# Performance work log

Measured on AMD Instinct MI355X. Metric: run time of the kernel, lower is better.

Reference implementation:

```python
import jax, jax.numpy as jnp
import numpy as np
from jax import lax

PATCH = 3
RBF_SIGMA = 0.06 * PATCH ** 2      # module scales sigma by patch_size**2
SIG2 = RBF_SIGMA ** 2


def _unfold(img):
    # torch.nn.Unfold(kernel_size=3, stride=1): (b, c*9, N) with N=(H-2)*(W-2).
    # Channel ordering inside d differs from torch but distances sum over d,
    # so any consistent patch flattening yields identical math.
    p = lax.conv_general_dilated_patches(img, (PATCH, PATCH), (1, 1), 'VALID')
    b, d = p.shape[0], p.shape[1]
    return p.reshape(b, d, -1)  # (b, d, N)


def _kernel_mean(xu, yu):
    # mean over (N, M) of exp(-||x_i - y_j||^2 / sigma^2), via the
    # ||x||^2 + ||y||^2 - 2<x,y> expansion (avoids the (b,d,N,M) diff tensor).
    sqx = jnp.sum(xu * xu, axis=1)                   # (b, N)
    sqy = jnp.sum(yu * yu, axis=1)                   # (b, M)
    gram = jnp.einsum('bdn,bdm->bnm', xu, yu)        # (b, N, M)
    d2 = sqx[:, :, None] + sqy[:, None, :] - 2.0 * gram
    return jnp.mean(jnp.exp(-d2 / SIG2), axis=(1, 2))  # (b,)


def setup_inputs() -> dict:
    key = jax.random.key(0)
    kx, ky = jax.random.split(key)
    x = jax.random.normal(kx, (8, 3, 64, 64), dtype=jnp.float32)
    y = jax.random.normal(ky, (8, 3, 64, 64), dtype=jnp.float32)
    return {"x": x, "y": y}


def reference(x, y):
    xu = _unfold(x)
    yu = _unfold(y)
    batch_loss = (-2.0 * _kernel_mean(xu, yu)
                  + _kernel_mean(xu, xu)
                  + _kernel_mean(yu, yu))       # (b,)
    return jnp.mean(batch_loss)                 # batch_reduction='mean'
```

## Files before the change

kernel.cpp:

```cpp
#include <hip/hip_runtime.h>
#include <hip/hip_bf16.h>


#define NP    3844
#define NPAD  3968
#define KP    32

#define W_XY  7688
#define W_ALL 15624
#define NBLK  15624

static constexpr float L_F   = 4.9475824173972215f;
static constexpr float C2L_F = 9.895164834794443f;

using bf16x8 = __attribute__((ext_vector_type(8))) short;
using f32x4  = __attribute__((ext_vector_type(4))) float;

#define MFMA16(a, b, c) __builtin_amdgcn_mfma_f32_16x16x32_bf16((a), (b), (c), 0, 0, 0)

__device__ inline unsigned short f2bf(float f) {
    union { float f; unsigned u; } v; v.f = f;
    unsigned r = v.u + 0x7FFFu + ((v.u >> 16) & 1u);
    return (unsigned short)(r >> 16);
}
__device__ inline float bf2f(unsigned short h) {
    union { unsigned u; float f; } v; v.u = ((unsigned)h) << 16;
    return v.f;
}
__device__ inline void pack_store(unsigned short* dst, const unsigned short* v) {
    uint4* d = (uint4*)dst;
#pragma unroll
    for (int q = 0; q < 4; ++q) {
        unsigned w0 = (unsigned)v[8 * q + 0] | ((unsigned)v[8 * q + 1] << 16);
        unsigned w1 = (unsigned)v[8 * q + 2] | ((unsigned)v[8 * q + 3] << 16);
        unsigned w2 = (unsigned)v[8 * q + 4] | ((unsigned)v[8 * q + 5] << 16);
        unsigned w3 = (unsigned)v[8 * q + 6] | ((unsigned)v[8 * q + 7] << 16);
        d[q] = make_uint4(w0, w1, w2, w3);
    }
}

__global__ __launch_bounds__(256) void gp_prep(const float* __restrict__ x,
                                               const float* __restrict__ y,
                                               unsigned short* __restrict__ Am,
                                               unsigned short* __restrict__ Bm) {
    int i = blockIdx.x * 256 + threadIdx.x;
    if (i >= 16 * NPAD) return;
    int n = i % NPAD, im = i / NPAD;
    int b = im & 7;
    const float* src = (im >> 3) ? y : x;

    const unsigned short ONE = f2bf(1.0f);
    unsigned short hA[32], hB[32];
#pragma unroll
    for (int k = 0; k < 32; ++k) { hA[k] = 0; hB[k] = 0; }

    if (n < NP) {
        int r = n / 62, c = n % 62;
        float s = 0.0f;
#pragma unroll
        for (int ch = 0; ch < 3; ++ch)
#pragma unroll
            for (int pr = 0; pr < 3; ++pr)
#pragma unroll
                for (int pc = 0; pc < 3; ++pc) {
                    int k = ch * 9 + pr * 3 + pc;
                    float v = src[(((b * 3 + ch) * 64) + r + pr) * 64 + (c + pc)];
                    unsigned short ah = f2bf(C2L_F * v);
                    unsigned short bh = f2bf(v);
                    hA[k] = ah; hB[k] = bh;
                    s = fmaf(bf2f(ah), bf2f(bh), s);
                }
        float p = -0.5f * s;
        hA[27] = f2bf(p); hA[28] = f2bf(p - bf2f(hA[27]));
        hA[29] = ONE; hA[30] = ONE;
        hB[27] = ONE; hB[28] = ONE;
        hB[29] = f2bf(p); hB[30] = f2bf(p - bf2f(hB[29]));
    } else {
        hA[27] = f2bf(-1e30f); hA[29] = ONE; hA[30] = ONE;
        hB[27] = ONE; hB[28] = ONE; hB[29] = f2bf(-1e30f);
    }

    pack_store(Am + (size_t)i * KP, hA);
    pack_store(Bm + (size_t)i * KP, hB);
}

template<int OFF>
__device__ inline bf16x8 gload(const unsigned short* p) {
    bf16x8 r;
    asm volatile("global_load_dwordx4 %0, %1, off offset:%2"
                 : "=v"(r) : "v"(p), "i"(OFF));
    return r;
}

#define BODY(BHC)                                                            \
    do {                                                                     \
        const f32x4 Z = {0.f, 0.f, 0.f, 0.f};                                \
        f32x4 g0 = MFMA16(ah0, BHC, Z); f32x4 g1 = MFMA16(ah1, BHC, Z);      \
        f32x4 g2 = MFMA16(ah2, BHC, Z); f32x4 g3 = MFMA16(ah3, BHC, Z);      \
        f32x4 g4 = MFMA16(ah4, BHC, Z); f32x4 g5 = MFMA16(ah5, BHC, Z);      \
        f32x4 g6 = MFMA16(ah6, BHC, Z); f32x4 g7 = MFMA16(ah7, BHC, Z);      \
        float m0 = fmaxf(fmaxf(fmaxf(g0[0], g0[1]), g0[2]), g0[3]);          \
        float m1 = fmaxf(fmaxf(fmaxf(g1[0], g1[1]), g1[2]), g1[3]);          \
        float m2 = fmaxf(fmaxf(fmaxf(g2[0], g2[1]), g2[2]), g2[3]);          \
        float m3 = fmaxf(fmaxf(fmaxf(g3[0], g3[1]), g3[2]), g3[3]);          \
        float m4 = fmaxf(fmaxf(fmaxf(g4[0], g4[1]), g4[2]), g4[3]);          \
        float m5 = fmaxf(fmaxf(fmaxf(g5[0], g5[1]), g5[2]), g5[3]);          \
        float m6 = fmaxf(fmaxf(fmaxf(g6[0], g6[1]), g6[2]), g6[3]);          \
        float m7 = fmaxf(fmaxf(fmaxf(g7[0], g7[1]), g7[2]), g7[3]);          \
        float mm = fmaxf(fmaxf(fmaxf(fmaxf(fmaxf(fmaxf(fmaxf(m0, m1), m2),   \
                         m3), m4), m5), m6), m7);                            \
        if (__any(mm > -40.0f)) {                                            \
            s0 += __builtin_amdgcn_exp2f(g0[0]); s1 += __builtin_amdgcn_exp2f(g0[1]); \
            s2 += __builtin_amdgcn_exp2f(g0[2]); s3 += __builtin_amdgcn_exp2f(g0[3]); \
            s0 += __builtin_amdgcn_exp2f(g1[0]); s1 += __builtin_amdgcn_exp2f(g1[1]); \
            s2 += __builtin_amdgcn_exp2f(g1[2]); s3 += __builtin_amdgcn_exp2f(g1[3]); \
            s0 += __builtin_amdgcn_exp2f(g2[0]); s1 += __builtin_amdgcn_exp2f(g2[1]); \
            s2 += __builtin_amdgcn_exp2f(g2[2]); s3 += __builtin_amdgcn_exp2f(g2[3]); \
            s0 += __builtin_amdgcn_exp2f(g3[0]); s1 += __builtin_amdgcn_exp2f(g3[1]); \
            s2 += __builtin_amdgcn_exp2f(g3[2]); s3 += __builtin_amdgcn_exp2f(g3[3]); \
            s0 += __builtin_amdgcn_exp2f(g4[0]); s1 += __builtin_amdgcn_exp2f(g4[1]); \
            s2 += __builtin_amdgcn_exp2f(g4[2]); s3 += __builtin_amdgcn_exp2f(g4[3]); \
            s0 += __builtin_amdgcn_exp2f(g5[0]); s1 += __builtin_amdgcn_exp2f(g5[1]); \
            s2 += __builtin_amdgcn_exp2f(g5[2]); s3 += __builtin_amdgcn_exp2f(g5[3]); \
            s0 += __builtin_amdgcn_exp2f(g6[0]); s1 += __builtin_amdgcn_exp2f(g6[1]); \
            s2 += __builtin_amdgcn_exp2f(g6[2]); s3 += __builtin_amdgcn_exp2f(g6[3]); \
            s0 += __builtin_amdgcn_exp2f(g7[0]); s1 += __builtin_amdgcn_exp2f(g7[1]); \
            s2 += __builtin_amdgcn_exp2f(g7[2]); s3 += __builtin_amdgcn_exp2f(g7[3]); \
        }                                                                    \
    } while (0)

#define STEPN(N, CURREG)                                                     \
    do {                                                                     \
        asm volatile("s_waitcnt vmcnt(" #N ")" : "+v"(CURREG));              \
        __builtin_amdgcn_sched_barrier(0);                                   \
        BODY(CURREG);                                                        \
    } while (0)

__global__ __launch_bounds__(64, 4) void gp_pairs21(const unsigned short* __restrict__ Am,
                                                    const unsigned short* __restrict__ Bm,
                                                    float* __restrict__ part) {
    const int phys = blockIdx.x;
    const int w = (phys & 7) * 1953 + (phys >> 3);

    const int l = threadIdx.x & 63;
    const int l15 = l & 15, lhi = l >> 4;

    int type, b, bx, by;
    float wt;
    if (w < W_XY) {
        type = 0; b = w / 961;
        int rr = w % 961; by = rr / 31; bx = rr % 31;
        wt = -2.0f;
    } else {
        int v = w - W_XY;
        type = 1 + v / 3968;
        int r = v % 3968; b = r / 496; int t2 = r % 496;
        by = (int)((sqrtf(8.0f * (float)t2 + 1.0f) - 1.0f) * 0.5f);
        while ((by + 1) * (by + 2) / 2 <= t2) ++by;
        while (by * (by + 1) / 2 > t2) --by;
        bx = t2 - by * (by + 1) / 2;
        wt = (bx == by) ? 1.0f : 2.0f;
    }
    int imA, imB;
    if (type == 0)      { imA = b;     imB = 8 + b; }
    else if (type == 1) { imA = b;     imB = b;     }
    else                { imA = 8 + b; imB = 8 + b; }

    const size_t eA = ((size_t)(imA * NPAD + bx * 128 + l15)) * KP + lhi * 8;
    const size_t eB = ((size_t)(imB * NPAD + by * 128 + l15)) * KP + lhi * 8;
    const unsigned short* pA0 = Am + eA;
    const unsigned short* pA4 = pA0 + 2048;
    const unsigned short* pB0 = Bm + eB;
    const unsigned short* pB4 = pB0 + 2048;

    bf16x8 ah0 = gload<0>(pA0),    ah1 = gload<1024>(pA0);
    bf16x8 ah2 = gload<2048>(pA0), ah3 = gload<3072>(pA0);
    bf16x8 ah4 = gload<0>(pA4),    ah5 = gload<1024>(pA4);
    bf16x8 ah6 = gload<2048>(pA4), ah7 = gload<3072>(pA4);

    bf16x8 b0 = gload<0>(pB0),    b1 = gload<1024>(pB0);
    bf16x8 b2 = gload<2048>(pB0), b3 = gload<3072>(pB0);
    bf16x8 b4 = gload<0>(pB4),    b5 = gload<1024>(pB4);
    bf16x8 b6 = gload<2048>(pB4), b7 = gload<3072>(pB4);

    asm volatile("s_waitcnt vmcnt(8)"
                 : "+v"(ah0), "+v"(ah1), "+v"(ah2), "+v"(ah3),
                   "+v"(ah4), "+v"(ah5), "+v"(ah6), "+v"(ah7));
    __builtin_amdgcn_sched_barrier(0);

    float s0 = 0.f, s1 = 0.f, s2 = 0.f, s3 = 0.f;

    STEPN(7, b0);
    STEPN(6, b1);
    STEPN(5, b2);
    STEPN(4, b3);
    STEPN(3, b4);
    STEPN(2, b5);
    STEPN(1, b6);
    STEPN(0, b7);

    float sacc = wt * ((s0 + s1) + (s2 + s3));

#pragma unroll
    for (int o = 32; o > 0; o >>= 1) sacc += __shfl_down(sacc, o, 64);
    if (l == 0) part[w] = sacc;
}

__global__ __launch_bounds__(1024) void gp_finish(const float* __restrict__ part,
                                                  float* __restrict__ out) {
    __shared__ float red[16];
    const int t = threadIdx.x;
    const int wv = t >> 6, l = t & 63;

    float s = 0.0f;
    for (int i = t; i < W_ALL; i += 1024) s += part[i];
#pragma unroll
    for (int o = 32; o > 0; o >>= 1) s += __shfl_down(s, o, 64);
    if (l == 0) red[wv] = s;
    __syncthreads();
    if (t == 0) {
        double d = 0.0;
#pragma unroll
        for (int i = 0; i < 16; ++i) d += (double)red[i];
        out[0] = (float)(d / (8.0 * (double)NP * (double)NP));
    }
}

extern "C" void kernel_launch(void* const* d_in, const int* in_sizes, int n_in,
                              void* d_out, int out_size, void* d_ws, size_t ws_size,
                              hipStream_t stream) {
    const float* x = (const float*)d_in[0];
    const float* y = (const float*)d_in[1];
    const size_t MSZ = (size_t)16 * NPAD * KP;
    unsigned short* Am = (unsigned short*)d_ws;
    unsigned short* Bm = Am + MSZ;
    float* part = (float*)(Bm + MSZ);

    gp_prep<<<(16 * NPAD) / 256, 256, 0, stream>>>(x, y, Am, Bm);
    gp_pairs21<<<NBLK, 64, 0, stream>>>(Am, Bm, part);
    gp_finish<<<1, 1024, 0, stream>>>(part, (float*)d_out);
}
```

Measured before the change: 40.13 us.

## Use 256x256 block tiles with B tile shared via LDS across four waves

Replaces the one-wave 128x128 tile kernel with a four-wave 256x256 tile kernel. Each wave holds a 64-row A slice in registers, and the 256-column B tile is loaded once into LDS with global_load_lds and shared by all waves. Padding grows to 4096 per image and the block count drops to 4224. This is meant to cut redundant global B loads and per-block scheduling overhead. In exchange it adds a block-wide barrier, LDS reads, more padded work, and coarser tiles that give fewer chances to skip tiles whose values are all negligible.

```diff
diff --git a/kernel.cpp b/kernel.cpp
--- a/kernel.cpp
+++ b/kernel.cpp
@@ -3,12 +3,11 @@
 
 
 #define NP    3844
-#define NPAD  3968
+#define NPAD  4096
 #define KP    32
 
-#define W_XY  7688
-#define W_ALL 15624
-#define NBLK  15624
+#define XYB   2048
+#define NBLK  4224
 
 static constexpr float L_F   = 4.9475824173972215f;
 static constexpr float C2L_F = 9.895164834794443f;
@@ -84,31 +83,22 @@
     pack_store(Bm + (size_t)i * KP, hB);
 }
 
-template<int OFF>
-__device__ inline bf16x8 gload(const unsigned short* p) {
-    bf16x8 r;
-    asm volatile("global_load_dwordx4 %0, %1, off offset:%2"
-                 : "=v"(r) : "v"(p), "i"(OFF));
-    return r;
-}
-
-#define BODY(BHC)                                                            \
+__device__ inline void glds(const unsigned short* p, char* lptr) {
+    __builtin_amdgcn_global_load_lds(
+        (const __attribute__((address_space(1))) void*)p,
+        (__attribute__((address_space(3))) void*)lptr, 16, 0, 0);
+}
+
+#define BODY4(BHC)                                                           \
     do {                                                                     \
         const f32x4 Z = {0.f, 0.f, 0.f, 0.f};                                \
         f32x4 g0 = MFMA16(ah0, BHC, Z); f32x4 g1 = MFMA16(ah1, BHC, Z);      \
         f32x4 g2 = MFMA16(ah2, BHC, Z); f32x4 g3 = MFMA16(ah3, BHC, Z);      \
-        f32x4 g4 = MFMA16(ah4, BHC, Z); f32x4 g5 = MFMA16(ah5, BHC, Z);      \
-        f32x4 g6 = MFMA16(ah6, BHC, Z); f32x4 g7 = MFMA16(ah7, BHC, Z);      \
         float m0 = fmaxf(fmaxf(fmaxf(g0[0], g0[1]), g0[2]), g0[3]);          \
         float m1 = fmaxf(fmaxf(fmaxf(g1[0], g1[1]), g1[2]), g1[3]);          \
         float m2 = fmaxf(fmaxf(fmaxf(g2[0], g2[1]), g2[2]), g2[3]);          \
         float m3 = fmaxf(fmaxf(fmaxf(g3[0], g3[1]), g3[2]), g3[3]);          \
-        float m4 = fmaxf(fmaxf(fmaxf(g4[0], g4[1]), g4[2]), g4[3]);          \
-        float m5 = fmaxf(fmaxf(fmaxf(g5[0], g5[1]), g5[2]), g5[3]);          \
-        float m6 = fmaxf(fmaxf(fmaxf(g6[0], g6[1]), g6[2]), g6[3]);          \
-        float m7 = fmaxf(fmaxf(fmaxf(g7[0], g7[1]), g7[2]), g7[3]);          \
-        float mm = fmaxf(fmaxf(fmaxf(fmaxf(fmaxf(fmaxf(fmaxf(m0, m1), m2),   \
-                         m3), m4), m5), m6), m7);                            \
+        float mm = fmaxf(fmaxf(fmaxf(m0, m1), m2), m3);                      \
         if (__any(mm > -40.0f)) {                                            \
             s0 += __builtin_amdgcn_exp2f(g0[0]); s1 += __builtin_amdgcn_exp2f(g0[1]); \
             s2 += __builtin_amdgcn_exp2f(g0[2]); s3 += __builtin_amdgcn_exp2f(g0[3]); \
@@ -118,92 +108,75 @@
             s2 += __builtin_amdgcn_exp2f(g2[2]); s3 += __builtin_amdgcn_exp2f(g2[3]); \
             s0 += __builtin_amdgcn_exp2f(g3[0]); s1 += __builtin_amdgcn_exp2f(g3[1]); \
             s2 += __builtin_amdgcn_exp2f(g3[2]); s3 += __builtin_amdgcn_exp2f(g3[3]); \
-            s0 += __builtin_amdgcn_exp2f(g4[0]); s1 += __builtin_amdgcn_exp2f(g4[1]); \
-            s2 += __builtin_amdgcn_exp2f(g4[2]); s3 += __builtin_amdgcn_exp2f(g4[3]); \
-            s0 += __builtin_amdgcn_exp2f(g5[0]); s1 += __builtin_amdgcn_exp2f(g5[1]); \
-            s2 += __builtin_amdgcn_exp2f(g5[2]); s3 += __builtin_amdgcn_exp2f(g5[3]); \
-            s0 += __builtin_amdgcn_exp2f(g6[0]); s1 += __builtin_amdgcn_exp2f(g6[1]); \
-            s2 += __builtin_amdgcn_exp2f(g6[2]); s3 += __builtin_amdgcn_exp2f(g6[3]); \
-            s0 += __builtin_amdgcn_exp2f(g7[0]); s1 += __builtin_amdgcn_exp2f(g7[1]); \
-            s2 += __builtin_amdgcn_exp2f(g7[2]); s3 += __builtin_amdgcn_exp2f(g7[3]); \
         }                                                                    \
     } while (0)
 
-#define STEPN(N, CURREG)                                                     \
-    do {                                                                     \
-        asm volatile("s_waitcnt vmcnt(" #N ")" : "+v"(CURREG));              \
-        __builtin_amdgcn_sched_barrier(0);                                   \
-        BODY(CURREG);                                                        \
-    } while (0)
-
-__global__ __launch_bounds__(64, 4) void gp_pairs21(const unsigned short* __restrict__ Am,
-                                                    const unsigned short* __restrict__ Bm,
-                                                    float* __restrict__ part) {
+__global__ __launch_bounds__(256, 4) void gp_pairs22(const unsigned short* __restrict__ Am,
+                                                     const unsigned short* __restrict__ Bm,
+                                                     float* __restrict__ part) {
+    __shared__ __align__(16) char ldsB[16384];
+    __shared__ float red[4];
+
     const int phys = blockIdx.x;
-    const int w = (phys & 7) * 1953 + (phys >> 3);
-
-    const int l = threadIdx.x & 63;
+    const int blk = (phys & 7) * 528 + (phys >> 3);
+
+    const int t = threadIdx.x;
+    const int wv = t >> 6, l = t & 63;
     const int l15 = l & 15, lhi = l >> 4;
 
-    int type, b, bx, by;
+    int type, b, si, sj;
     float wt;
-    if (w < W_XY) {
-        type = 0; b = w / 961;
-        int rr = w % 961; by = rr / 31; bx = rr % 31;
+    if (blk < XYB) {
+        type = 0; b = blk >> 8;
+        int rr = blk & 255; si = rr >> 4; sj = rr & 15;
         wt = -2.0f;
     } else {
-        int v = w - W_XY;
-        type = 1 + v / 3968;
-        int r = v % 3968; b = r / 496; int t2 = r % 496;
-        by = (int)((sqrtf(8.0f * (float)t2 + 1.0f) - 1.0f) * 0.5f);
-        while ((by + 1) * (by + 2) / 2 <= t2) ++by;
-        while (by * (by + 1) / 2 > t2) --by;
-        bx = t2 - by * (by + 1) / 2;
-        wt = (bx == by) ? 1.0f : 2.0f;
+        int id2 = blk - XYB;
+        type = 1 + id2 / 1088;
+        int r = id2 % 1088; b = r / 136; int t2 = r % 136;
+        sj = (int)((sqrtf(8.0f * (float)t2 + 1.0f) - 1.0f) * 0.5f);
+        while ((sj + 1) * (sj + 2) / 2 <= t2) ++sj;
+        while (sj * (sj + 1) / 2 > t2) --sj;
+        si = t2 - sj * (sj + 1) / 2;
+        wt = (si == sj) ? 1.0f : 2.0f;
     }
     int imA, imB;
     if (type == 0)      { imA = b;     imB = 8 + b; }
     else if (type == 1) { imA = b;     imB = b;     }
     else                { imA = 8 + b; imB = 8 + b; }
 
-    const size_t eA = ((size_t)(imA * NPAD + bx * 128 + l15)) * KP + lhi * 8;
-    const size_t eB = ((size_t)(imB * NPAD + by * 128 + l15)) * KP + lhi * 8;
-    const unsigned short* pA0 = Am + eA;
-    const unsigned short* pA4 = pA0 + 2048;
-    const unsigned short* pB0 = Bm + eB;
-    const unsigned short* pB4 = pB0 + 2048;
-
-    bf16x8 ah0 = gload<0>(pA0),    ah1 = gload<1024>(pA0);
-    bf16x8 ah2 = gload<2048>(pA0), ah3 = gload<3072>(pA0);
-    bf16x8 ah4 = gload<0>(pA4),    ah5 = gload<1024>(pA4);
-    bf16x8 ah6 = gload<2048>(pA4), ah7 = gload<3072>(pA4);
-
-    bf16x8 b0 = gload<0>(pB0),    b1 = gload<1024>(pB0);
-    bf16x8 b2 = gload<2048>(pB0), b3 = gload<3072>(pB0);
-    bf16x8 b4 = gload<0>(pB4),    b5 = gload<1024>(pB4);
-    bf16x8 b6 = gload<2048>(pB4), b7 = gload<3072>(pB4);
-
-    asm volatile("s_waitcnt vmcnt(8)"
-                 : "+v"(ah0), "+v"(ah1), "+v"(ah2), "+v"(ah3),
-                   "+v"(ah4), "+v"(ah5), "+v"(ah6), "+v"(ah7));
-    __builtin_amdgcn_sched_barrier(0);
+    const size_t eA = ((size_t)(imA * NPAD + si * 256 + wv * 64 + l15)) * KP + lhi * 8;
+    const unsigned short* pA = Am + eA;
+    bf16x8 ah0 = *(const bf16x8*)(pA);
+    bf16x8 ah1 = *(const bf16x8*)(pA + 512);
+    bf16x8 ah2 = *(const bf16x8*)(pA + 1024);
+    bf16x8 ah3 = *(const bf16x8*)(pA + 1536);
+    asm volatile("" : "+v"(ah0), "+v"(ah1), "+v"(ah2), "+v"(ah3));
+
+#pragma unroll
+    for (int j = 0; j < 4; ++j) {
+        const int q = wv * 4 + j;
+        const unsigned short* src = Bm
+            + ((size_t)(imB * NPAD + sj * 256 + q * 16 + l15)) * KP + lhi * 8;
+        glds(src, ldsB + q * 1024);
+    }
+    __syncthreads();
 
     float s0 = 0.f, s1 = 0.f, s2 = 0.f, s3 = 0.f;
 
-    STEPN(7, b0);
-    STEPN(6, b1);
-    STEPN(5, b2);
-    STEPN(4, b3);
-    STEPN(3, b4);
-    STEPN(2, b5);
-    STEPN(1, b6);
-    STEPN(0, b7);
-
-    float sacc = wt * ((s0 + s1) + (s2 + s3));
+#pragma unroll
+    for (int cg = 0; cg < 16; ++cg) {
+        const bf16x8 bhc = *(const bf16x8*)(ldsB + cg * 1024 + l * 16);
+        BODY4(bhc);
+    }
+
+    float sacc = (s0 + s1) + (s2 + s3);
 
 #pragma unroll
     for (int o = 32; o > 0; o >>= 1) sacc += __shfl_down(sacc, o, 64);
-    if (l == 0) part[w] = sacc;
+    if (l == 0) red[wv] = sacc;
+    __syncthreads();
+    if (t == 0) part[blk] = wt * ((red[0] + red[1]) + (red[2] + red[3]));
 }
 
 __global__ __launch_bounds__(1024) void gp_finish(const float* __restrict__ part,
@@ -213,7 +186,7 @@
     const int wv = t >> 6, l = t & 63;
 
     float s = 0.0f;
-    for (int i = t; i < W_ALL; i += 1024) s += part[i];
+    for (int i = t; i < NBLK; i += 1024) s += part[i];
 #pragma unroll
     for (int o = 32; o > 0; o >>= 1) s += __shfl_down(s, o, 64);
     if (l == 0) red[wv] = s;
@@ -237,6 +210,6 @@
     float* part = (float*)(Bm + MSZ);
 
     gp_prep<<<(16 * NPAD) / 256, 256, 0, stream>>>(x, y, Am, Bm);
-    gp_pairs21<<<NBLK, 64, 0, stream>>>(Am, Bm, part);
+    gp_pairs22<<<NBLK, 256, 0, stream>>>(Am, Bm, part);
     gp_finish<<<1, 1024, 0, stream>>>(part, (float*)d_out);
 }
```

Measured after the change: 37.07 us. -7.6%, faster.
